# Kernel optimization log

Hardware: AMD Instinct MI355X
Metric: run time of the kernel (lower is better)

## Reference

```python
import jax, jax.numpy as jnp
import numpy as np
import math

HEADS = 4
LN_EPS = 1e-5


def _layer_norm(x, gamma, beta):
    # LayerNorm over last dim (N=4096), matching nn.LayerNorm(4096)
    mu = jnp.mean(x, axis=-1, keepdims=True)
    var = jnp.mean((x - mu) ** 2, axis=-1, keepdims=True)
    return (x - mu) * jax.lax.rsqrt(var + LN_EPS) * gamma + beta


def setup_inputs() -> dict:
    key = jax.random.key(0)
    ks = jax.random.split(key, 10)
    L, IMG, N = 1024, 1024, 4096
    s_img = 1.0 / math.sqrt(IMG)
    s_L = 1.0 / math.sqrt(L)
    return {
        "point_features": jax.random.normal(ks[0], (1, L, N), jnp.float32),
        "img_features": jax.random.normal(ks[1], (1, IMG, N), jnp.float32),
        # 4 per-head 1x1 convs IMG_chl -> L_chl
        "W_img": jax.random.normal(ks[2], (HEADS, L, IMG), jnp.float32) * s_img,
        "b_img": jax.random.normal(ks[3], (HEADS, L), jnp.float32) * s_img,
        # conv_L: L_chl -> L_chl
        "W_L": jax.random.normal(ks[4], (L, L), jnp.float32) * s_L,
        "b_L": jax.random.normal(ks[5], (L,), jnp.float32) * s_L,
        # LayerNorm(4096)
        "ln_g": jnp.ones((N,), jnp.float32),
        "ln_b": jnp.zeros((N,), jnp.float32),
        # conv_fusion: L_chl -> L_chl
        "W_f": jax.random.normal(ks[6], (L, L), jnp.float32) * s_L,
        "b_f": jax.random.normal(ks[7], (L,), jnp.float32) * s_L,
    }


def reference(point_features, img_features, W_img, b_img, W_L, b_L, ln_g, ln_b, W_f, b_f):
    # L_query = conv_L(point_features): [1, L, N]
    L_query = jnp.einsum('oi,bin->bon', W_L, point_features) + b_L[None, :, None]
    dk = L_query.shape[1]
    N = L_query.shape[2]

    # All 4 head keys at once: [H, 1, L, N]
    keys = jnp.einsum('hoi,bin->hbon', W_img, img_features) + b_img[:, None, :, None]

    # score_i = sum_c(key_i * query) / sqrt(dk)  -> cat over heads: [H, N] (B=1)
    score = jnp.sum(keys * L_query[None], axis=2).reshape(HEADS, N) / jnp.sqrt(jnp.float32(dk))

    # softmax across heads (dim=0), weightmap = [1, H, N]
    weight = jax.nn.softmax(score, axis=0)
    weightmap = weight[None]

    # z = sum_h weight[h] * key_h : [1, L, N]
    z = jnp.einsum('hn,hbcn->bcn', weight, keys)

    fused = _layer_norm(z + L_query, ln_g, ln_b)
    fusion_features = jnp.einsum('oi,bin->bon', W_f, fused) + b_f[None, :, None]
    return (fusion_features, weightmap)
```

## Files before the change

kernel.cpp:

```cpp
#include <hip/hip_runtime.h>
#include <hip/hip_bf16.h>
#include <stdint.h>

using u16 = unsigned short;

typedef __attribute__((ext_vector_type(8))) short bf16x8;
typedef __attribute__((ext_vector_type(4))) float f32x4;

typedef const __attribute__((address_space(1))) unsigned int* gas_t;
typedef __attribute__((address_space(3))) unsigned int* las_t;

__device__ inline void g2l16(const u16* g, u16* l) {
  __builtin_amdgcn_global_load_lds((gas_t)g, (las_t)l, 16, 0, 0);
}

__device__ inline u16 f2b(float x) {
  union { float f; uint32_t u; } v; v.f = x;
  uint32_t r = (v.u + 0x7FFFu + ((v.u >> 16) & 1u)) >> 16;
  return (u16)r;
}
__device__ inline float b2f(u16 b) {
  union { uint32_t u; float f; } v; v.u = ((uint32_t)b) << 16;
  return v.f;
}
__device__ inline float b2f_lo(uint32_t p) { 
  union { uint32_t u; float f; } v; v.u = p << 16; return v.f;
}
__device__ inline float b2f_hi(uint32_t p) {
  union { uint32_t u; float f; } v; v.u = p & 0xFFFF0000u; return v.f;
}

__device__ inline void store_out(float* p, float v) { *p = v; }
__device__ inline void store_out(u16* p, float v) { *p = f2b(v); }

template<typename OutT>
__global__ __launch_bounds__(256)
void gemm_bt(const u16* __restrict__ A, const u16* __restrict__ Bt,
             const float* __restrict__ bias, OutT* __restrict__ C,
             int M, int N, int K)
{
  __shared__ u16 As[128 * 64];
  __shared__ u16 Bs[128 * 64];

  const int tid  = threadIdx.x;
  const int wave = tid >> 6;
  const int lane = tid & 63;
  const int wm = wave >> 1, wn = wave & 1;
  const int lr = lane & 15;
  const int lq = lane >> 4;
  const int x7 = lr & 7;

  const int m0 = blockIdx.y * 128;
  const int n0 = blockIdx.x * 128;

  const int srow = tid >> 3;
  const int sgc  = (tid & 7) ^ (srow & 7);
  const u16* gA = A  + (size_t)(m0 + srow) * K + sgc * 8;
  const u16* gB = Bt + (size_t)(n0 + srow) * K + sgc * 8;
  u16* dstA = As + wave * 512;
  u16* dstB = Bs + wave * 512;

  f32x4 acc[4][4];
  #pragma unroll
  for (int i = 0; i < 4; ++i)
    #pragma unroll
    for (int j = 0; j < 4; ++j)
      acc[i][j] = (f32x4){0.f, 0.f, 0.f, 0.f};

  for (int k0 = 0; k0 < K; k0 += 64) {
    #pragma unroll
    for (int s = 0; s < 4; ++s) {
      g2l16(gA + (size_t)(s * 32) * K + k0, dstA + s * 2048);
      g2l16(gB + (size_t)(s * 32) * K + k0, dstB + s * 2048);
    }
    __syncthreads();

    #pragma unroll
    for (int ks = 0; ks < 2; ++ks) {
      const int pa = (ks * 4 + lq) ^ x7;
      bf16x8 af[4], bfr[4];
      #pragma unroll
      for (int im = 0; im < 4; ++im)
        af[im] = *(const bf16x8*)&As[(wm * 64 + im * 16 + lr) * 64 + pa * 8];
      #pragma unroll
      for (int in = 0; in < 4; ++in)
        bfr[in] = *(const bf16x8*)&Bs[(wn * 64 + in * 16 + lr) * 64 + pa * 8];

      #pragma unroll
      for (int im = 0; im < 4; ++im)
        #pragma unroll
        for (int in = 0; in < 4; ++in)
          acc[im][in] = __builtin_amdgcn_mfma_f32_16x16x32_bf16(
              af[im], bfr[in], acc[im][in], 0, 0, 0);
    }
    __syncthreads();
  }

  #pragma unroll
  for (int im = 0; im < 4; ++im) {
    const int mbase = m0 + wm * 64 + im * 16 + lq * 4;
    #pragma unroll
    for (int in = 0; in < 4; ++in) {
      const int ncol = n0 + wn * 64 + in * 16 + lr;
      #pragma unroll
      for (int r = 0; r < 4; ++r) {
        const int m = mbase + r;
        store_out(C + (size_t)m * N + ncol, acc[im][in][r] + bias[m]);
      }
    }
  }
}

template<typename OutT>
__global__ __launch_bounds__(256)
void gemm_bt_64(const u16* __restrict__ A, const u16* __restrict__ Bt,
                const float* __restrict__ bias, OutT* __restrict__ C,
                int M, int N, int K)
{
  __shared__ u16 As[64 * 64];
  __shared__ u16 Bs[128 * 64];

  const int tid  = threadIdx.x;
  const int wave = tid >> 6;
  const int lane = tid & 63;
  const int lr = lane & 15;
  const int lq = lane >> 4;
  const int x7 = lr & 7;

  const int m0 = blockIdx.y * 64;
  const int n0 = blockIdx.x * 128;

  const int srow = tid >> 3;
  const int sgc  = (tid & 7) ^ (srow & 7);
  const u16* gA = A  + (size_t)(m0 + srow) * K + sgc * 8;
  const u16* gB = Bt + (size_t)(n0 + srow) * K + sgc * 8;
  u16* dstA = As + wave * 512;
  u16* dstB = Bs + wave * 512;

  f32x4 acc[4][2];
  #pragma unroll
  for (int i = 0; i < 4; ++i)
    #pragma unroll
    for (int j = 0; j < 2; ++j)
      acc[i][j] = (f32x4){0.f, 0.f, 0.f, 0.f};

  for (int k0 = 0; k0 < K; k0 += 64) {
    #pragma unroll
    for (int s = 0; s < 2; ++s)
      g2l16(gA + (size_t)(s * 32) * K + k0, dstA + s * 2048);
    #pragma unroll
    for (int s = 0; s < 4; ++s)
      g2l16(gB + (size_t)(s * 32) * K + k0, dstB + s * 2048);
    __syncthreads();

    #pragma unroll
    for (int ks = 0; ks < 2; ++ks) {
      const int pa = (ks * 4 + lq) ^ x7;
      bf16x8 af[4], bfr[2];
      #pragma unroll
      for (int im = 0; im < 4; ++im)
        af[im] = *(const bf16x8*)&As[(im * 16 + lr) * 64 + pa * 8];
      #pragma unroll
      for (int in = 0; in < 2; ++in)
        bfr[in] = *(const bf16x8*)&Bs[(wave * 32 + in * 16 + lr) * 64 + pa * 8];

      #pragma unroll
      for (int im = 0; im < 4; ++im)
        #pragma unroll
        for (int in = 0; in < 2; ++in)
          acc[im][in] = __builtin_amdgcn_mfma_f32_16x16x32_bf16(
              af[im], bfr[in], acc[im][in], 0, 0, 0);
    }
    __syncthreads();
  }

  #pragma unroll
  for (int im = 0; im < 4; ++im) {
    const int mbase = m0 + im * 16 + lq * 4;
    #pragma unroll
    for (int in = 0; in < 2; ++in) {
      const int ncol = n0 + wave * 32 + in * 16 + lr;
      #pragma unroll
      for (int r = 0; r < 4; ++r) {
        const int m = mbase + r;
        store_out(C + (size_t)m * N + ncol, acc[im][in][r] + bias[m]);
      }
    }
  }
}

__global__ __launch_bounds__(256)
void cast_transpose2(const float* __restrict__ in0, u16* __restrict__ out0,
                     const float* __restrict__ in1, u16* __restrict__ out1,
                     int R, int C)
{
  const float* in = blockIdx.z ? in1 : in0;
  u16* out = blockIdx.z ? out1 : out0;
  __shared__ u16 tile[32][33];
  const int c0 = blockIdx.x * 32, r0 = blockIdx.y * 32;
  const int tx = threadIdx.x & 31, ty = threadIdx.x >> 5;
  #pragma unroll
  for (int k = 0; k < 4; ++k)
    tile[ty + 8 * k][tx] = f2b(in[(size_t)(r0 + ty + 8 * k) * C + c0 + tx]);
  __syncthreads();
  #pragma unroll
  for (int k = 0; k < 4; ++k)
    out[(size_t)(c0 + ty + 8 * k) * R + r0 + tx] = tile[tx][ty + 8 * k];
}

__global__ __launch_bounds__(256)
void transpose_u16(const u16* __restrict__ in, u16* __restrict__ out,
                   int R, int C)
{
  __shared__ u16 tile[32][33];
  const int c0 = blockIdx.x * 32, r0 = blockIdx.y * 32;
  const int tx = threadIdx.x & 31, ty = threadIdx.x >> 5;
  #pragma unroll
  for (int k = 0; k < 4; ++k)
    tile[ty + 8 * k][tx] = in[(size_t)(r0 + ty + 8 * k) * C + c0 + tx];
  __syncthreads();
  #pragma unroll
  for (int k = 0; k < 4; ++k)
    out[(size_t)(c0 + ty + 8 * k) * R + r0 + tx] = tile[tx][ty + 8 * k];
}

__global__ __launch_bounds__(256)
void cast_weights(const float4* __restrict__ wim, const float4* __restrict__ wl,
                  const float4* __restrict__ wf, ushort4* __restrict__ wimb,
                  ushort4* __restrict__ wlb, ushort4* __restrict__ wfb)
{
  int i = blockIdx.x * 256 + threadIdx.x;
  const float4* src; ushort4* dst;
  if (i < 1048576)      { src = wim; dst = wimb; }
  else if (i < 1310720) { src = wl;  dst = wlb;  i -= 1048576; }
  else                  { src = wf;  dst = wfb;  i -= 1310720; }
  const float4 v = src[i];
  ushort4 o;
  o.x = f2b(v.x); o.y = f2b(v.y); o.z = f2b(v.z); o.w = f2b(v.w);
  dst[i] = o;
}

__global__ __launch_bounds__(256)
void score_partial(const u16* __restrict__ keys, const u16* __restrict__ Qb,
                   float* __restrict__ spart)
{
  const int n  = blockIdx.x * 256 + threadIdx.x;
  const int cb = blockIdx.y;
  const int c0 = cb * 32;
  float s[4] = {0.f, 0.f, 0.f, 0.f};
  #pragma unroll 8
  for (int c = c0; c < c0 + 32; ++c) {
    const float q = b2f(Qb[(size_t)c * 4096 + n]);
    #pragma unroll
    for (int h = 0; h < 4; ++h)
      s[h] = fmaf(q, b2f(keys[((size_t)((h << 10) + c)) * 4096 + n]), s[h]);
  }
  #pragma unroll
  for (int h = 0; h < 4; ++h)
    spart[((size_t)cb * 4 + h) * 4096 + n] = s[h];
}

__global__ __launch_bounds__(256)
void softmax_h(const float* __restrict__ spart, float* __restrict__ wmap)
{
  const int n = blockIdx.x * 256 + threadIdx.x;
  float s[4] = {0.f, 0.f, 0.f, 0.f};
  for (int cb = 0; cb < 32; ++cb)
    #pragma unroll
    for (int h = 0; h < 4; ++h)
      s[h] += spart[((size_t)cb * 4 + h) * 4096 + n];
  #pragma unroll
  for (int h = 0; h < 4; ++h) s[h] *= 0.03125f;
  const float m = fmaxf(fmaxf(s[0], s[1]), fmaxf(s[2], s[3]));
  const float e0 = expf(s[0] - m), e1 = expf(s[1] - m);
  const float e2 = expf(s[2] - m), e3 = expf(s[3] - m);
  const float inv = 1.f / (e0 + e1 + e2 + e3);
  wmap[n] = e0 * inv; wmap[4096 + n] = e1 * inv;
  wmap[8192 + n] = e2 * inv; wmap[12288 + n] = e3 * inv;
}

__global__ __launch_bounds__(256)
void z_ln(const u16* __restrict__ keys, const u16* __restrict__ Qb,
          const float* __restrict__ w, const float* __restrict__ g,
          const float* __restrict__ bb, u16* __restrict__ fused)
{
  const int c  = blockIdx.x;
  const int tx = threadIdx.x;
  float t[16];
  float s = 0.f, s2 = 0.f;
  #pragma unroll
  for (int j = 0; j < 8; ++j) {
    const int n = tx * 2 + j * 512;
    const uint32_t qv = *(const uint32_t*)&Qb[(size_t)c * 4096 + n];
    float z0 = 0.f, z1 = 0.f;
    #pragma unroll
    for (int h = 0; h < 4; ++h) {
      const uint32_t kv = *(const uint32_t*)&keys[((size_t)((h << 10) + c)) * 4096 + n];
      const float2 wv = *(const float2*)&w[h * 4096 + n];
      z0 = fmaf(wv.x, b2f_lo(kv), z0);
      z1 = fmaf(wv.y, b2f_hi(kv), z1);
    }
    const float v0 = z0 + b2f_lo(qv);
    const float v1 = z1 + b2f_hi(qv);
    t[2 * j] = v0; t[2 * j + 1] = v1;
    s += v0 + v1;
    s2 = fmaf(v0, v0, fmaf(v1, v1, s2));
  }
  #pragma unroll
  for (int o = 32; o > 0; o >>= 1) {
    s  += __shfl_down(s, o);
    s2 += __shfl_down(s2, o);
  }
  __shared__ float rbuf[8];
  const int wave = tx >> 6, lane = tx & 63;
  if (lane == 0) { rbuf[wave] = s; rbuf[4 + wave] = s2; }
  __syncthreads();
  s  = rbuf[0] + rbuf[1] + rbuf[2] + rbuf[3];
  s2 = rbuf[4] + rbuf[5] + rbuf[6] + rbuf[7];
  const float mu  = s * (1.f / 4096.f);
  const float var = s2 * (1.f / 4096.f) - mu * mu;
  const float rs  = rsqrtf(var + 1e-5f);
  #pragma unroll
  for (int j = 0; j < 8; ++j) {
    const int n = tx * 2 + j * 512;
    const float2 gv = *(const float2*)&g[n];
    const float2 bv = *(const float2*)&bb[n];
    const u16 o0 = f2b((t[2 * j]     - mu) * rs * gv.x + bv.x);
    const u16 o1 = f2b((t[2 * j + 1] - mu) * rs * gv.y + bv.y);
    *(uint32_t*)&fused[(size_t)c * 4096 + n] = ((uint32_t)o1 << 16) | o0;
  }
}

extern "C" void kernel_launch(void* const* d_in, const int* in_sizes, int n_in,
                              void* d_out, int out_size, void* d_ws, size_t ws_size,
                              hipStream_t stream)
{
  const float* P   = (const float*)d_in[0];
  const float* I   = (const float*)d_in[1];
  const float* Wim = (const float*)d_in[2];
  const float* bim = (const float*)d_in[3];
  const float* WL  = (const float*)d_in[4];
  const float* bL  = (const float*)d_in[5];
  const float* lng = (const float*)d_in[6];
  const float* lnb = (const float*)d_in[7];
  const float* Wf  = (const float*)d_in[8];
  const float* bf_ = (const float*)d_in[9];
  float* out = (float*)d_out;

  char* ws = (char*)d_ws;
  u16*   PT     = (u16*)(ws + 0);
  u16*   IT     = (u16*)(ws + (size_t)8  * 1048576);
  u16*   WLb    = (u16*)(ws + (size_t)16 * 1048576);
  u16*   WIb    = (u16*)(ws + (size_t)18 * 1048576);
  u16*   WFb    = (u16*)(ws + (size_t)26 * 1048576);
  u16*   Qb     = (u16*)(ws + (size_t)28 * 1048576);
  u16*   KEYS   = (u16*)(ws + (size_t)36 * 1048576);
  float* SPART  = (float*)(ws + (size_t)68 * 1048576);
  u16*   FUSED  = (u16*)(ws + (size_t)70 * 1048576);
  u16*   FUSEDT = (u16*)(ws + (size_t)78 * 1048576);

  const dim3 b256(256);

  cast_transpose2<<<dim3(128, 32, 2), b256, 0, stream>>>(P, PT, I, IT, 1024, 4096);
  cast_weights<<<6144, b256, 0, stream>>>((const float4*)Wim, (const float4*)WL,
                                          (const float4*)Wf, (ushort4*)WIb,
                                          (ushort4*)WLb, (ushort4*)WFb);

  gemm_bt_64<u16><<<dim3(32, 16), b256, 0, stream>>>(WLb, PT, bL, Qb, 1024, 4096, 1024);
  gemm_bt<u16><<<dim3(32, 32), b256, 0, stream>>>(WIb, IT, bim, KEYS, 4096, 4096, 1024);

  score_partial<<<dim3(16, 32), b256, 0, stream>>>(KEYS, Qb, SPART);
  float* wmap = out + (size_t)1024 * 4096;
  softmax_h<<<16, b256, 0, stream>>>(SPART, wmap);

  z_ln<<<1024, b256, 0, stream>>>(KEYS, Qb, wmap, lng, lnb, FUSED);
  transpose_u16<<<dim3(128, 32), b256, 0, stream>>>(FUSED, FUSEDT, 1024, 4096);

  gemm_bt_64<float><<<dim3(32, 16), b256, 0, stream>>>(WFb, FUSEDT, bf_, out, 1024, 4096, 1024);
}
```

Baseline: 256.8 us.

## Merge query and key GEMMs into one launch and widen memory accesses

The query GEMM and the four-head key GEMM now share a single launch, with block rows 32-39 running the 128x128 tile path on the query problem, so both fill the GPU together instead of running as two separate grids. The transpose kernels drop their shared-memory tiles: each thread loads a 4x4 block with vector loads and writes transposed 4-wide vectors. score_partial handles two columns per thread and z_ln four, using wider loads and stores. The register transposes give up the coalescing of the shared-memory version on the strided writes, and the merged GEMM uses 128-row tiles for the query problem.

```diff
diff --git a/kernel.cpp b/kernel.cpp
--- a/kernel.cpp
+++ b/kernel.cpp
@@ -23,7 +23,7 @@
   union { uint32_t u; float f; } v; v.u = ((uint32_t)b) << 16;
   return v.f;
 }
-__device__ inline float b2f_lo(uint32_t p) { 
+__device__ inline float b2f_lo(uint32_t p) {
   union { uint32_t u; float f; } v; v.u = p << 16; return v.f;
 }
 __device__ inline float b2f_hi(uint32_t p) {
@@ -34,14 +34,13 @@
 __device__ inline void store_out(u16* p, float v) { *p = f2b(v); }
 
 template<typename OutT>
-__global__ __launch_bounds__(256)
-void gemm_bt(const u16* __restrict__ A, const u16* __restrict__ Bt,
-             const float* __restrict__ bias, OutT* __restrict__ C,
-             int M, int N, int K)
-{
-  __shared__ u16 As[128 * 64];
-  __shared__ u16 Bs[128 * 64];
-
+__device__ inline void gemm_tile_128(const u16* __restrict__ A,
+                                     const u16* __restrict__ Bt,
+                                     const float* __restrict__ bias,
+                                     OutT* __restrict__ C,
+                                     int m0, int n0, int N, int K,
+                                     u16* As, u16* Bs)
+{
   const int tid  = threadIdx.x;
   const int wave = tid >> 6;
   const int lane = tid & 63;
@@ -50,9 +49,6 @@
   const int lq = lane >> 4;
   const int x7 = lr & 7;
 
-  const int m0 = blockIdx.y * 128;
-  const int n0 = blockIdx.x * 128;
-
   const int srow = tid >> 3;
   const int sgc  = (tid & 7) ^ (srow & 7);
   const u16* gA = A  + (size_t)(m0 + srow) * K + sgc * 8;
@@ -111,6 +107,22 @@
   }
 }
 
+__global__ __launch_bounds__(256)
+void gemm_dual(const u16* __restrict__ WIb, const u16* __restrict__ IT,
+               const float* __restrict__ bim, u16* __restrict__ KEYS,
+               const u16* __restrict__ WLb, const u16* __restrict__ PT,
+               const float* __restrict__ bL, u16* __restrict__ Qb)
+{
+  __shared__ u16 As[128 * 64];
+  __shared__ u16 Bs[128 * 64];
+  const int by = blockIdx.y;
+  const int n0 = blockIdx.x * 128;
+  if (by < 32)
+    gemm_tile_128<u16>(WIb, IT, bim, KEYS, by * 128, n0, 4096, 1024, As, Bs);
+  else
+    gemm_tile_128<u16>(WLb, PT, bL, Qb, (by - 32) * 128, n0, 4096, 1024, As, Bs);
+}
+
 template<typename OutT>
 __global__ __launch_bounds__(256)
 void gemm_bt_64(const u16* __restrict__ A, const u16* __restrict__ Bt,
@@ -196,32 +208,40 @@
 {
   const float* in = blockIdx.z ? in1 : in0;
   u16* out = blockIdx.z ? out1 : out0;
-  __shared__ u16 tile[32][33];
-  const int c0 = blockIdx.x * 32, r0 = blockIdx.y * 32;
-  const int tx = threadIdx.x & 31, ty = threadIdx.x >> 5;
-  #pragma unroll
-  for (int k = 0; k < 4; ++k)
-    tile[ty + 8 * k][tx] = f2b(in[(size_t)(r0 + ty + 8 * k) * C + c0 + tx]);
-  __syncthreads();
-  #pragma unroll
-  for (int k = 0; k < 4; ++k)
-    out[(size_t)(c0 + ty + 8 * k) * R + r0 + tx] = tile[tx][ty + 8 * k];
+  const int c0 = blockIdx.x * 64 + (threadIdx.x & 15) * 4;
+  const int r0 = blockIdx.y * 64 + (threadIdx.x >> 4) * 4;
+  float4 v[4];
+  #pragma unroll
+  for (int i = 0; i < 4; ++i)
+    v[i] = *(const float4*)&in[(size_t)(r0 + i) * C + c0];
+  const float* f = (const float*)v;
+  #pragma unroll
+  for (int j = 0; j < 4; ++j) {
+    ushort4 o;
+    o.x = f2b(f[0 * 4 + j]); o.y = f2b(f[1 * 4 + j]);
+    o.z = f2b(f[2 * 4 + j]); o.w = f2b(f[3 * 4 + j]);
+    *(ushort4*)&out[(size_t)(c0 + j) * R + r0] = o;
+  }
 }
 
 __global__ __launch_bounds__(256)
 void transpose_u16(const u16* __restrict__ in, u16* __restrict__ out,
                    int R, int C)
 {
-  __shared__ u16 tile[32][33];
-  const int c0 = blockIdx.x * 32, r0 = blockIdx.y * 32;
-  const int tx = threadIdx.x & 31, ty = threadIdx.x >> 5;
-  #pragma unroll
-  for (int k = 0; k < 4; ++k)
-    tile[ty + 8 * k][tx] = in[(size_t)(r0 + ty + 8 * k) * C + c0 + tx];
-  __syncthreads();
-  #pragma unroll
-  for (int k = 0; k < 4; ++k)
-    out[(size_t)(c0 + ty + 8 * k) * R + r0 + tx] = tile[tx][ty + 8 * k];
+  const int c0 = blockIdx.x * 64 + (threadIdx.x & 15) * 4;
+  const int r0 = blockIdx.y * 64 + (threadIdx.x >> 4) * 4;
+  ushort4 v[4];
+  #pragma unroll
+  for (int i = 0; i < 4; ++i)
+    v[i] = *(const ushort4*)&in[(size_t)(r0 + i) * C + c0];
+  const u16* e = (const u16*)v;
+  #pragma unroll
+  for (int j = 0; j < 4; ++j) {
+    ushort4 o;
+    o.x = e[0 * 4 + j]; o.y = e[1 * 4 + j];
+    o.z = e[2 * 4 + j]; o.w = e[3 * 4 + j];
+    *(ushort4*)&out[(size_t)(c0 + j) * R + r0] = o;
+  }
 }
 
 __global__ __launch_bounds__(256)
@@ -244,20 +264,26 @@
 void score_partial(const u16* __restrict__ keys, const u16* __restrict__ Qb,
                    float* __restrict__ spart)
 {
-  const int n  = blockIdx.x * 256 + threadIdx.x;
+  const int n  = (blockIdx.x * 256 + threadIdx.x) * 2;
   const int cb = blockIdx.y;
   const int c0 = cb * 32;
-  float s[4] = {0.f, 0.f, 0.f, 0.f};
+  float2 s[4];
+  #pragma unroll
+  for (int h = 0; h < 4; ++h) s[h] = make_float2(0.f, 0.f);
   #pragma unroll 8
   for (int c = c0; c < c0 + 32; ++c) {
-    const float q = b2f(Qb[(size_t)c * 4096 + n]);
-    #pragma unroll
-    for (int h = 0; h < 4; ++h)
-      s[h] = fmaf(q, b2f(keys[((size_t)((h << 10) + c)) * 4096 + n]), s[h]);
+    const uint32_t qv = *(const uint32_t*)&Qb[(size_t)c * 4096 + n];
+    const float q0 = b2f_lo(qv), q1 = b2f_hi(qv);
+    #pragma unroll
+    for (int h = 0; h < 4; ++h) {
+      const uint32_t kv = *(const uint32_t*)&keys[((size_t)((h << 10) + c)) * 4096 + n];
+      s[h].x = fmaf(q0, b2f_lo(kv), s[h].x);
+      s[h].y = fmaf(q1, b2f_hi(kv), s[h].y);
+    }
   }
   #pragma unroll
   for (int h = 0; h < 4; ++h)
-    spart[((size_t)cb * 4 + h) * 4096 + n] = s[h];
+    *(float2*)&spart[((size_t)cb * 4 + h) * 4096 + n] = s[h];
 }
 
 __global__ __launch_bounds__(256)
@@ -289,22 +315,26 @@
   float t[16];
   float s = 0.f, s2 = 0.f;
   #pragma unroll
-  for (int j = 0; j < 8; ++j) {
-    const int n = tx * 2 + j * 512;
-    const uint32_t qv = *(const uint32_t*)&Qb[(size_t)c * 4096 + n];
-    float z0 = 0.f, z1 = 0.f;
+  for (int j = 0; j < 4; ++j) {
+    const int n = tx * 4 + j * 1024;
+    const uint2 qv = *(const uint2*)&Qb[(size_t)c * 4096 + n];
+    float z0 = 0.f, z1 = 0.f, z2 = 0.f, z3 = 0.f;
     #pragma unroll
     for (int h = 0; h < 4; ++h) {
-      const uint32_t kv = *(const uint32_t*)&keys[((size_t)((h << 10) + c)) * 4096 + n];
-      const float2 wv = *(const float2*)&w[h * 4096 + n];
-      z0 = fmaf(wv.x, b2f_lo(kv), z0);
-      z1 = fmaf(wv.y, b2f_hi(kv), z1);
-    }
-    const float v0 = z0 + b2f_lo(qv);
-    const float v1 = z1 + b2f_hi(qv);
-    t[2 * j] = v0; t[2 * j + 1] = v1;
-    s += v0 + v1;
-    s2 = fmaf(v0, v0, fmaf(v1, v1, s2));
+      const uint2 kv = *(const uint2*)&keys[((size_t)((h << 10) + c)) * 4096 + n];
+      const float4 wv = *(const float4*)&w[h * 4096 + n];
+      z0 = fmaf(wv.x, b2f_lo(kv.x), z0);
+      z1 = fmaf(wv.y, b2f_hi(kv.x), z1);
+      z2 = fmaf(wv.z, b2f_lo(kv.y), z2);
+      z3 = fmaf(wv.w, b2f_hi(kv.y), z3);
+    }
+    const float v0 = z0 + b2f_lo(qv.x);
+    const float v1 = z1 + b2f_hi(qv.x);
+    const float v2 = z2 + b2f_lo(qv.y);
+    const float v3 = z3 + b2f_hi(qv.y);
+    t[4 * j] = v0; t[4 * j + 1] = v1; t[4 * j + 2] = v2; t[4 * j + 3] = v3;
+    s += (v0 + v1) + (v2 + v3);
+    s2 = fmaf(v0, v0, fmaf(v1, v1, fmaf(v2, v2, fmaf(v3, v3, s2))));
   }
   #pragma unroll
   for (int o = 32; o > 0; o >>= 1) {
@@ -321,13 +351,16 @@
   const float var = s2 * (1.f / 4096.f) - mu * mu;
   const float rs  = rsqrtf(var + 1e-5f);
   #pragma unroll
-  for (int j = 0; j < 8; ++j) {
-    const int n = tx * 2 + j * 512;
-    const float2 gv = *(const float2*)&g[n];
-    const float2 bv = *(const float2*)&bb[n];
-    const u16 o0 = f2b((t[2 * j]     - mu) * rs * gv.x + bv.x);
-    const u16 o1 = f2b((t[2 * j + 1] - mu) * rs * gv.y + bv.y);
-    *(uint32_t*)&fused[(size_t)c * 4096 + n] = ((uint32_t)o1 << 16) | o0;
+  for (int j = 0; j < 4; ++j) {
+    const int n = tx * 4 + j * 1024;
+    const float4 gv = *(const float4*)&g[n];
+    const float4 bv = *(const float4*)&bb[n];
+    ushort4 o;
+    o.x = f2b((t[4 * j]     - mu) * rs * gv.x + bv.x);
+    o.y = f2b((t[4 * j + 1] - mu) * rs * gv.y + bv.y);
+    o.z = f2b((t[4 * j + 2] - mu) * rs * gv.z + bv.z);
+    o.w = f2b((t[4 * j + 3] - mu) * rs * gv.w + bv.w);
+    *(ushort4*)&fused[(size_t)c * 4096 + n] = o;
   }
 }
 
@@ -361,20 +394,19 @@
 
   const dim3 b256(256);
 
-  cast_transpose2<<<dim3(128, 32, 2), b256, 0, stream>>>(P, PT, I, IT, 1024, 4096);
+  cast_transpose2<<<dim3(64, 16, 2), b256, 0, stream>>>(P, PT, I, IT, 1024, 4096);
   cast_weights<<<6144, b256, 0, stream>>>((const float4*)Wim, (const float4*)WL,
                                           (const float4*)Wf, (ushort4*)WIb,
                                           (ushort4*)WLb, (ushort4*)WFb);
 
-  gemm_bt_64<u16><<<dim3(32, 16), b256, 0, stream>>>(WLb, PT, bL, Qb, 1024, 4096, 1024);
-  gemm_bt<u16><<<dim3(32, 32), b256, 0, stream>>>(WIb, IT, bim, KEYS, 4096, 4096, 1024);
-
-  score_partial<<<dim3(16, 32), b256, 0, stream>>>(KEYS, Qb, SPART);
+  gemm_dual<<<dim3(32, 40), b256, 0, stream>>>(WIb, IT, bim, KEYS, WLb, PT, bL, Qb);
+
+  score_partial<<<dim3(8, 32), b256, 0, stream>>>(KEYS, Qb, SPART);
   float* wmap = out + (size_t)1024 * 4096;
   softmax_h<<<16, b256, 0, stream>>>(SPART, wmap);
 
   z_ln<<<1024, b256, 0, stream>>>(KEYS, Qb, wmap, lng, lnb, FUSED);
-  transpose_u16<<<dim3(128, 32), b256, 0, stream>>>(FUSED, FUSEDT, 1024, 4096);
+  transpose_u16<<<dim3(64, 16), b256, 0, stream>>>(FUSED, FUSEDT, 1024, 4096);
 
   gemm_bt_64<float><<<dim3(32, 16), b256, 0, stream>>>(WFb, FUSEDT, bf_, out, 1024, 4096, 1024);
 }
```

After: 291.9 us. +13.7%, slower.
